# Kernel tuning notes

Hardware: AMD Instinct MI355X
Metric: run time of the kernel (lower is better)

## Reference

```python
import jax, jax.numpy as jnp
import numpy as np

N = 100000


def gcn_conv(x, edge_index, W, b):
    """PyG GCNConv: add self-loops, symmetric normalization, x @ W, aggregate, + bias."""
    n = x.shape[0]
    src = jnp.concatenate([edge_index[0], jnp.arange(n)])
    dst = jnp.concatenate([edge_index[1], jnp.arange(n)])
    deg = jax.ops.segment_sum(jnp.ones_like(dst, dtype=x.dtype), dst, num_segments=n)
    dinv = jnp.where(deg > 0, jax.lax.rsqrt(deg), 0.0)
    norm = dinv[src] * dinv[dst]  # [E+N]
    h = x @ W  # [N, out]
    msg = h[src] * norm[:, None]  # gather + scale
    agg = jax.ops.segment_sum(msg, dst, num_segments=n)
    return agg + b


def setup_inputs() -> dict:
    key = jax.random.key(0)
    ks = jax.random.split(key, 10)
    x = jax.random.normal(ks[0], (N, 256), dtype=jnp.float32)
    edge_index = jax.random.randint(ks[1], (2, 3200000), 0, N, dtype=jnp.int64)
    def glorot(k, fan_in, fan_out):
        s = np.sqrt(6.0 / (fan_in + fan_out)).astype(np.float32)
        return jax.random.uniform(k, (fan_in, fan_out), jnp.float32, -s, s)
    return {
        "x": x,
        "edge_index": edge_index,
        "W1": glorot(ks[2], 256, 128), "b1": jnp.zeros((128,), jnp.float32),
        "W2": glorot(ks[3], 128, 64), "b2": jnp.zeros((64,), jnp.float32),
        "W3": glorot(ks[4], 64, 16), "b3": jnp.zeros((16,), jnp.float32),
        "Wc": glorot(ks[5], 16, 2), "bc": jnp.zeros((2,), jnp.float32),
    }


def reference(x, edge_index, W1, b1, W2, b2, W3, b3, Wc, bc):
    h = jnp.tanh(gcn_conv(x, edge_index, W1, b1))
    h = jnp.tanh(gcn_conv(h, edge_index, W2, b2))
    h = jnp.tanh(gcn_conv(h, edge_index, W3, b3))
    out = h @ Wc + bc
    return (out, h)
```

## Files before the change

### kernel.cpp

```cpp
#include <hip/hip_runtime.h>
#include <hip/hip_fp16.h>
#include <cstdint>
#include <cstddef>


#define EPB 16384
#define BSHIFT 8
#define NBUC_MAX 512
#define BCAP 12800

typedef __attribute__((ext_vector_type(8))) short short8;
typedef __attribute__((ext_vector_type(4))) float f32x4;

__global__ __launch_bounds__(256) void scan_block(const int* __restrict__ src, int n,
                                                  int* __restrict__ incl,
                                                  int* __restrict__ bsum) {
    int tid = threadIdx.x;
    int v = blockIdx.x * 256 + tid;
    int val = (v < n) ? src[v] : 0;
    int lane = tid & 63, w = tid >> 6;
#pragma unroll
    for (int off = 1; off < 64; off <<= 1) {
        int t = __shfl_up(val, off, 64);
        if (lane >= off) val += t;
    }
    __shared__ int wsum[4];
    if (lane == 63) wsum[w] = val;
    __syncthreads();
#pragma unroll
    for (int i = 0; i < 4; ++i)
        if (i < w) val += wsum[i];
    if (v < n) incl[v] = val;
    if (tid == 255) bsum[blockIdx.x] = val;
}

__global__ __launch_bounds__(512) void scan_sums(int* __restrict__ bsum, int nb) {
    int tid = threadIdx.x;
    int val = (tid < nb) ? bsum[tid] : 0;
    int lane = tid & 63, w = tid >> 6;
#pragma unroll
    for (int off = 1; off < 64; off <<= 1) {
        int t = __shfl_up(val, off, 64);
        if (lane >= off) val += t;
    }
    __shared__ int wsum[8];
    if (lane == 63) wsum[w] = val;
    __syncthreads();
#pragma unroll
    for (int i = 0; i < 8; ++i)
        if (i < w) val += wsum[i];
    if (tid < nb) bsum[tid] = val;
}

__global__ __launch_bounds__(256) void finalize_scan(
    const int* __restrict__ incl, const int* __restrict__ bsum,
    const int* __restrict__ src, int n, int* __restrict__ excl) {
    int v = blockIdx.x * 256 + threadIdx.x;
    if (v >= n) return;
    int boff = (blockIdx.x == 0) ? 0 : bsum[blockIdx.x - 1];
    excl[v] = boff + incl[v] - src[v];
}

__global__ __launch_bounds__(256) void hist_bucket(
    const int* __restrict__ ei, int E, int nbuc, int nch,
    int* __restrict__ histG) {
    __shared__ int h[NBUC_MAX];
    const int k = blockIdx.x;
    for (int b = threadIdx.x; b < NBUC_MAX; b += 256) h[b] = 0;
    __syncthreads();
    const int base = k * EPB, end = min(E, base + EPB);
    for (int i = base + threadIdx.x; i < end; i += 256)
        atomicAdd(&h[ei[(size_t)E + i] >> BSHIFT], 1);
    __syncthreads();
    for (int b = threadIdx.x; b < nbuc; b += 256)
        histG[(size_t)b * nch + k] = h[b];
}

__global__ __launch_bounds__(256) void bucket_scatter(
    const int* __restrict__ ei, int E, int nbuc, int nch,
    const int* __restrict__ offs, unsigned int* __restrict__ ebuf) {
    __shared__ int cur[NBUC_MAX];
    const int k = blockIdx.x;
    for (int b = threadIdx.x; b < nbuc; b += 256)
        cur[b] = offs[(size_t)b * nch + k];
    __syncthreads();
    const int base = k * EPB, end = min(E, base + EPB);
    for (int i = base + threadIdx.x; i < end; i += 256) {
        int s = ei[i];
        int d = ei[(size_t)E + i];
        int pos = atomicAdd(&cur[d >> BSHIFT], 1);
        ebuf[pos] = (unsigned)s | ((unsigned)(d & 255) << 24);
    }
}

__global__ __launch_bounds__(256) void bucket_build(
    const unsigned int* __restrict__ ebuf, const int* __restrict__ offs,
    int E, int nbuc, int nch, int n,
    int* __restrict__ col, int* __restrict__ deg,
    int* __restrict__ row_start, float* __restrict__ dinv) {
    const int b = blockIdx.x;
    const int tid = threadIdx.x;
    const int estart = offs[(size_t)b * nch];
    const int eend = (b + 1 < nbuc) ? offs[(size_t)(b + 1) * nch] : E;
    const int cnt = eend - estart;

    __shared__ int degl[256];
    __shared__ int curl[256];
    __shared__ int wsum[4];
    __shared__ int colstage[BCAP];

    degl[tid] = 0;
    __syncthreads();
    for (int i = tid; i < cnt; i += 256)
        atomicAdd(&degl[ebuf[estart + i] >> 24], 1);
    __syncthreads();
    int myDeg = degl[tid];
    int val = myDeg;
    int lane = tid & 63, w = tid >> 6;
#pragma unroll
    for (int off = 1; off < 64; off <<= 1) {
        int t = __shfl_up(val, off, 64);
        if (lane >= off) val += t;
    }
    if (lane == 63) wsum[w] = val;
    __syncthreads();
#pragma unroll
    for (int i = 0; i < 4; ++i)
        if (i < w) val += wsum[i];
    int excl = val - myDeg;
    curl[tid] = excl;
    int v = (b << BSHIFT) + tid;
    if (v < n) {
        deg[v] = myDeg;
        row_start[v] = estart + excl;
        dinv[v] = rsqrtf((float)(myDeg + 1));
    }
    __syncthreads();
    if (cnt <= BCAP) {
        for (int i = tid; i < cnt; i += 256) {
            unsigned int e = ebuf[estart + i];
            int pos = atomicAdd(&curl[e >> 24], 1);
            colstage[pos] = (int)(e & 0xFFFFFFu);
        }
        __syncthreads();
        for (int i = tid; i < cnt; i += 256)
            col[estart + i] = colstage[i];
    } else {
        for (int i = tid; i < cnt; i += 256) {
            unsigned int e = ebuf[estart + i];
            int pos = atomicAdd(&curl[e >> 24], 1);
            col[estart + pos] = (int)(e & 0xFFFFFFu);
        }
    }
}

__device__ inline unsigned short f32_to_bf16_rn(float f) {
    unsigned int u = __float_as_uint(f);
    unsigned int r = (u + 0x7FFFu + ((u >> 16) & 1u)) >> 16;
    return (unsigned short)r;
}
__device__ inline float bf16_to_f32(unsigned short h) {
    return __uint_as_float(((unsigned int)h) << 16);
}

template <int FIN, int FOUT>
__global__ __launch_bounds__(256) void pack_w(const float* __restrict__ W,
                                              unsigned short* __restrict__ Wpk) {
    constexpr int KC = FIN / 32, CF = FOUT / 16;
    constexpr int TOT = KC * CF * 64 * 8;
    int idx = blockIdx.x * 256 + threadIdx.x;
    if (idx >= TOT) return;
    int j = idx & 7;
    int lane = (idx >> 3) & 63;
    int cf = (idx >> 9) % CF;
    int kc = (idx >> 9) / CF;
    int k = kc * 32 + ((lane >> 4) * 8) + j;
    int c = cf * 16 + (lane & 15);
    float w = W[(size_t)k * FOUT + c];
    unsigned short h = f32_to_bf16_rn(w);
    unsigned short l = f32_to_bf16_rn(w - bf16_to_f32(h));
    size_t base = ((size_t)((kc * CF + cf) * 64 + lane)) * 16;
    Wpk[base + j] = h;
    Wpk[base + 8 + j] = l;
}

template <int FIN, int FOUT>
__global__ __launch_bounds__(256) void gemm_mfma(
    const float* __restrict__ X, const unsigned short* __restrict__ Wpk,
    const float* __restrict__ dinv, __half* __restrict__ Hs, int n) {
    constexpr int KC = FIN / 32, CF = FOUT / 16;
    constexpr int BM = 4 * 16;
    const int w = threadIdx.x >> 6, lane = threadIdx.x & 63;
    const int g = lane >> 4, rr = lane & 15;
    const int node0 = blockIdx.x * BM + w * 16;
    const int ko = g * 8;

    f32x4 acc[CF];
#pragma unroll
    for (int cf = 0; cf < CF; ++cf)
        acc[cf] = (f32x4){0.f, 0.f, 0.f, 0.f};

    union U16 { uint4 u; short8 s; };

#pragma unroll 2
    for (int kc = 0; kc < KC; ++kc) {
        short8 ahi, alo;
        {
            int r = node0 + rr;
            float xv[8] = {0.f, 0.f, 0.f, 0.f, 0.f, 0.f, 0.f, 0.f};
            if (r < n) {
                const float* xp = X + (size_t)r * FIN + kc * 32 + ko;
                float4 a0 = *(const float4*)xp;
                float4 a1 = *(const float4*)(xp + 4);
                xv[0] = a0.x; xv[1] = a0.y; xv[2] = a0.z; xv[3] = a0.w;
                xv[4] = a1.x; xv[5] = a1.y; xv[6] = a1.z; xv[7] = a1.w;
            }
#pragma unroll
            for (int j = 0; j < 8; ++j) {
                unsigned int u = __float_as_uint(xv[j]);
                ahi[j] = (short)(unsigned short)(u >> 16);
                float hf = __uint_as_float(u & 0xFFFF0000u);
                alo[j] = (short)f32_to_bf16_rn(xv[j] - hf);
            }
        }
#pragma unroll
        for (int cf = 0; cf < CF; ++cf) {
            const uint4* bp = (const uint4*)(Wpk +
                ((size_t)((kc * CF + cf) * 64 + lane)) * 16);
            U16 bh, bl;
            bh.u = bp[0];
            bl.u = bp[1];
            acc[cf] = __builtin_amdgcn_mfma_f32_16x16x32_bf16(
                ahi, bh.s, acc[cf], 0, 0, 0);
            acc[cf] = __builtin_amdgcn_mfma_f32_16x16x32_bf16(
                alo, bh.s, acc[cf], 0, 0, 0);
            acc[cf] = __builtin_amdgcn_mfma_f32_16x16x32_bf16(
                ahi, bl.s, acc[cf], 0, 0, 0);
        }
    }

#pragma unroll
    for (int i = 0; i < 4; ++i) {
        int r = node0 + g * 4 + i;
        if (r >= n) continue;
        float di = dinv[r];
        __half* hp = Hs + (size_t)r * FOUT + rr;
#pragma unroll
        for (int cf = 0; cf < CF; ++cf)
            hp[cf * 16] = __float2half_rn(acc[cf][i] * di);
    }
}

template <int FIN, int FOUT, int TM>
__global__ __launch_bounds__(256) void gemm_tile_h(
    const float* __restrict__ X, const float* __restrict__ W,
    const float* __restrict__ dinv, __half* __restrict__ Hs, int n) {
    constexpr int CT = FOUT / 4;
    constexpr int RG = 256 / CT;
    static_assert(TM == RG * 4, "tile mismatch");
    constexpr int LROW = FIN + 4;
    __shared__ float xs[TM][LROW];

    const int node0 = blockIdx.x * TM;
    const int tid = threadIdx.x;

    constexpr int C4 = FIN / 4;
    for (int i = tid; i < TM * C4; i += 256) {
        int r = i / C4, c = (i % C4) * 4;
        float4 v = make_float4(0.f, 0.f, 0.f, 0.f);
        if (node0 + r < n) v = *(const float4*)(X + (size_t)(node0 + r) * FIN + c);
        *(float4*)&xs[r][c] = v;
    }
    __syncthreads();

    const int col = (tid % CT) * 4;
    const int r0 = (tid / CT) * 4;

    float acc[4][4];
#pragma unroll
    for (int i = 0; i < 4; ++i)
#pragma unroll
        for (int j = 0; j < 4; ++j) acc[i][j] = 0.f;

#pragma unroll 2
    for (int k = 0; k < FIN; k += 4) {
        float4 w0 = *(const float4*)(W + (size_t)(k + 0) * FOUT + col);
        float4 w1 = *(const float4*)(W + (size_t)(k + 1) * FOUT + col);
        float4 w2 = *(const float4*)(W + (size_t)(k + 2) * FOUT + col);
        float4 w3 = *(const float4*)(W + (size_t)(k + 3) * FOUT + col);
        float4 av[4];
        av[0] = *(const float4*)&xs[r0 + 0][k];
        av[1] = *(const float4*)&xs[r0 + 1][k];
        av[2] = *(const float4*)&xs[r0 + 2][k];
        av[3] = *(const float4*)&xs[r0 + 3][k];
#pragma unroll
        for (int rr = 0; rr < 4; ++rr) {
            acc[rr][0] = fmaf(av[rr].x, w0.x, acc[rr][0]);
            acc[rr][1] = fmaf(av[rr].x, w0.y, acc[rr][1]);
            acc[rr][2] = fmaf(av[rr].x, w0.z, acc[rr][2]);
            acc[rr][3] = fmaf(av[rr].x, w0.w, acc[rr][3]);
            acc[rr][0] = fmaf(av[rr].y, w1.x, acc[rr][0]);
            acc[rr][1] = fmaf(av[rr].y, w1.y, acc[rr][1]);
            acc[rr][2] = fmaf(av[rr].y, w1.z, acc[rr][2]);
            acc[rr][3] = fmaf(av[rr].y, w1.w, acc[rr][3]);
            acc[rr][0] = fmaf(av[rr].z, w2.x, acc[rr][0]);
            acc[rr][1] = fmaf(av[rr].z, w2.y, acc[rr][1]);
            acc[rr][2] = fmaf(av[rr].z, w2.z, acc[rr][2]);
            acc[rr][3] = fmaf(av[rr].z, w2.w, acc[rr][3]);
            acc[rr][0] = fmaf(av[rr].w, w3.x, acc[rr][0]);
            acc[rr][1] = fmaf(av[rr].w, w3.y, acc[rr][1]);
            acc[rr][2] = fmaf(av[rr].w, w3.z, acc[rr][2]);
            acc[rr][3] = fmaf(av[rr].w, w3.w, acc[rr][3]);
        }
    }

#pragma unroll
    for (int rr = 0; rr < 4; ++rr) {
        int node = node0 + r0 + rr;
        if (node < n) {
            float di = dinv[node];
            __half h0 = __float2half_rn(acc[rr][0] * di);
            __half h1 = __float2half_rn(acc[rr][1] * di);
            __half h2 = __float2half_rn(acc[rr][2] * di);
            __half h3 = __float2half_rn(acc[rr][3] * di);
            unsigned short u0 = *(unsigned short*)&h0, u1 = *(unsigned short*)&h1;
            unsigned short u2 = *(unsigned short*)&h2, u3 = *(unsigned short*)&h3;
            uint2 pk;
            pk.x = (unsigned)u0 | ((unsigned)u1 << 16);
            pk.y = (unsigned)u2 | ((unsigned)u3 << 16);
            *(uint2*)(Hs + (size_t)node * FOUT + col) = pk;
        }
    }
}

__device__ inline void add8h(float* acc, uint4 p) {
    unsigned int w[4] = {p.x, p.y, p.z, p.w};
#pragma unroll
    for (int t = 0; t < 4; ++t) {
        __half2 h = *(const __half2*)&w[t];
        float2 f = __half22float2(h);
        acc[2 * t] += f.x;
        acc[2 * t + 1] += f.y;
    }
}

template <int F>
__global__ __launch_bounds__(256) void pull_agg_h(
    const int* __restrict__ row_start, const int* __restrict__ deg,
    const int* __restrict__ col, const __half* __restrict__ Hs,
    const float* __restrict__ dinv, const float* __restrict__ B,
    float* __restrict__ OUT, int n) {
    constexpr int TPE = F / 8;
    long long gid = (long long)blockIdx.x * 256 + threadIdx.x;
    int node = (int)(gid / TPE);
    int lane = (int)(gid % TPE);
    if (node >= n) return;
    const int beg = row_start[node];
    const int cnt = deg[node];
    const size_t lo = (size_t)lane * 8;

    float acc[8] = {0.f, 0.f, 0.f, 0.f, 0.f, 0.f, 0.f, 0.f};
    add8h(acc, *(const uint4*)(Hs + (size_t)node * F + lo));

    int j = 0;
    for (; j + 16 <= cnt; j += 16) {
        int s[16];
#pragma unroll
        for (int t = 0; t < 16; ++t) s[t] = col[beg + j + t];
        uint4 p[16];
#pragma unroll
        for (int t = 0; t < 16; ++t)
            p[t] = *(const uint4*)(Hs + (size_t)s[t] * F + lo);
#pragma unroll
        for (int t = 0; t < 16; ++t) add8h(acc, p[t]);
    }
    for (; j + 8 <= cnt; j += 8) {
        int s[8];
#pragma unroll
        for (int t = 0; t < 8; ++t) s[t] = col[beg + j + t];
        uint4 p[8];
#pragma unroll
        for (int t = 0; t < 8; ++t)
            p[t] = *(const uint4*)(Hs + (size_t)s[t] * F + lo);
#pragma unroll
        for (int t = 0; t < 8; ++t) add8h(acc, p[t]);
    }
    for (; j < cnt; ++j) {
        int s = col[beg + j];
        add8h(acc, *(const uint4*)(Hs + (size_t)s * F + lo));
    }

    float di = dinv[node];
    float4 b0 = *(const float4*)(B + lo);
    float4 b1 = *(const float4*)(B + lo + 4);
    float4 r0, r1;
    r0.x = tanhf(fmaf(acc[0], di, b0.x));
    r0.y = tanhf(fmaf(acc[1], di, b0.y));
    r0.z = tanhf(fmaf(acc[2], di, b0.z));
    r0.w = tanhf(fmaf(acc[3], di, b0.w));
    r1.x = tanhf(fmaf(acc[4], di, b1.x));
    r1.y = tanhf(fmaf(acc[5], di, b1.y));
    r1.z = tanhf(fmaf(acc[6], di, b1.z));
    r1.w = tanhf(fmaf(acc[7], di, b1.w));
    float* op = OUT + (size_t)node * F + lo;
    *(float4*)(op) = r0;
    *(float4*)(op + 4) = r1;
}

__global__ __launch_bounds__(256) void pull_cls(
    const int* __restrict__ row_start, const int* __restrict__ deg,
    const int* __restrict__ col, const __half* __restrict__ Hs,
    const float* __restrict__ dinv, const float* __restrict__ B,
    const float* __restrict__ Wc, const float* __restrict__ bc,
    float* __restrict__ OUTH, float* __restrict__ OUTC, int n) {
    int gid = blockIdx.x * 256 + threadIdx.x;
    int node = gid >> 1;
    if (node >= n) return;
    const int half = gid & 1;
    const size_t lo = (size_t)half * 8;
    const int beg = row_start[node];
    const int cnt = deg[node];

    float acc[8] = {0.f, 0.f, 0.f, 0.f, 0.f, 0.f, 0.f, 0.f};
    add8h(acc, *(const uint4*)(Hs + (size_t)node * 16 + lo));

    int j = 0;
    for (; j + 16 <= cnt; j += 16) {
        int s[16];
#pragma unroll
        for (int t = 0; t < 16; ++t) s[t] = col[beg + j + t];
        uint4 p[16];
#pragma unroll
        for (int t = 0; t < 16; ++t)
            p[t] = *(const uint4*)(Hs + (size_t)s[t] * 16 + lo);
#pragma unroll
        for (int t = 0; t < 16; ++t) add8h(acc, p[t]);
    }
    for (; j + 8 <= cnt; j += 8) {
        int s[8];
#pragma unroll
        for (int t = 0; t < 8; ++t) s[t] = col[beg + j + t];
        uint4 p[8];
#pragma unroll
        for (int t = 0; t < 8; ++t)
            p[t] = *(const uint4*)(Hs + (size_t)s[t] * 16 + lo);
#pragma unroll
        for (int t = 0; t < 8; ++t) add8h(acc, p[t]);
    }
    for (; j < cnt; ++j) {
        int s = col[beg + j];
        add8h(acc, *(const uint4*)(Hs + (size_t)s * 16 + lo));
    }

    float di = dinv[node];
    float r[8];
#pragma unroll
    for (int k = 0; k < 8; ++k)
        r[k] = tanhf(fmaf(acc[k], di, B[lo + k]));

    float* op = OUTH + (size_t)node * 16 + lo;
    *(float4*)(op)     = make_float4(r[0], r[1], r[2], r[3]);
    *(float4*)(op + 4) = make_float4(r[4], r[5], r[6], r[7]);

    float o0 = 0.f, o1 = 0.f;
#pragma unroll
    for (int k = 0; k < 8; ++k) {
        o0 = fmaf(r[k], Wc[(lo + k) * 2 + 0], o0);
        o1 = fmaf(r[k], Wc[(lo + k) * 2 + 1], o1);
    }
    o0 += __shfl_xor(o0, 1);
    o1 += __shfl_xor(o1, 1);
    if (half == 0) {
        OUTC[(size_t)node * 2 + 0] = o0 + bc[0];
        OUTC[(size_t)node * 2 + 1] = o1 + bc[1];
    }
}

extern "C" void kernel_launch(void* const* d_in, const int* in_sizes, int n_in,
                              void* d_out, int out_size, void* d_ws, size_t ws_size,
                              hipStream_t stream) {
    const float* x  = (const float*)d_in[0];
    const int* ei   = (const int*)d_in[1];
    const float* W1 = (const float*)d_in[2];
    const float* b1 = (const float*)d_in[3];
    const float* W2 = (const float*)d_in[4];
    const float* b2 = (const float*)d_in[5];
    const float* W3 = (const float*)d_in[6];
    const float* b3 = (const float*)d_in[7];
    const float* Wc = (const float*)d_in[8];
    const float* bc = (const float*)d_in[9];

    const int n = in_sizes[0] / 256;
    const int E = in_sizes[1] / 2;
    const int nbuc = (n + 255) >> BSHIFT;
    const int nch  = (E + EPB - 1) / EPB;
    const int NH   = nbuc * nch;
    const int nb2  = (NH + 255) / 256;

    float* outp = (float*)d_out;
    float* outh = outp + (size_t)n * 2;

    int*    deg       = (int*)d_ws;
    float*  dinv      = (float*)d_ws + (size_t)n;
    int*    row_start = (int*)d_ws + 2 * (size_t)n;
    int*    histG     = (int*)d_ws + 3 * (size_t)n;
    int*    incl      = histG + NH;
    int*    bsum      = incl + NH;
    int*    offs      = bsum + 512;
    int*    col       = offs + NH;
    __half* HsH       = (__half*)(col + E);
    float*  xbuf      = (float*)(HsH + (size_t)n * 128);
    unsigned int* ebuf = (unsigned int*)xbuf;

    unsigned short* Wpk1 = (unsigned short*)histG;
    unsigned short* Wpk2 = Wpk1 + (size_t)256 * 128 * 2;

    hist_bucket<<<nch, 256, 0, stream>>>(ei, E, nbuc, nch, histG);
    scan_block<<<nb2, 256, 0, stream>>>(histG, NH, incl, bsum);
    scan_sums<<<1, 512, 0, stream>>>(bsum, nb2);
    finalize_scan<<<nb2, 256, 0, stream>>>(incl, bsum, histG, NH, offs);
    bucket_scatter<<<nch, 256, 0, stream>>>(ei, E, nbuc, nch, offs, ebuf);
    bucket_build<<<nbuc, 256, 0, stream>>>(ebuf, offs, E, nbuc, nch, n,
                                           col, deg, row_start, dinv);

    pack_w<256, 128><<<(256 / 32 * 128 / 16 * 512 + 255) / 256, 256, 0, stream>>>(W1, Wpk1);
    pack_w<128, 64><<<(128 / 32 * 64 / 16 * 512 + 255) / 256, 256, 0, stream>>>(W2, Wpk2);

    gemm_mfma<256, 128><<<(n + 63) / 64, 256, 0, stream>>>(x, Wpk1, dinv, HsH, n);
    pull_agg_h<128><<<(int)(((long long)n * 16 + 255) / 256), 256, 0, stream>>>(
        row_start, deg, col, HsH, dinv, b1, xbuf, n);

    gemm_mfma<128, 64><<<(n + 63) / 64, 256, 0, stream>>>(xbuf, Wpk2, dinv, HsH, n);
    pull_agg_h<64><<<(int)(((long long)n * 8 + 255) / 256), 256, 0, stream>>>(
        row_start, deg, col, HsH, dinv, b2, xbuf, n);

    gemm_tile_h<64, 16, 256><<<(n + 255) / 256, 256, 0, stream>>>(xbuf, W3, dinv, HsH, n);
    pull_cls<<<(2 * n + 255) / 256, 256, 0, stream>>>(row_start, deg, col, HsH,
                                                      dinv, b3, Wc, bc, outh, outp, n);
}
```

Before: 634.7 us.

## Sort CSR neighbors and aggregate in source-column chunks for gather locality

Each node's neighbor list is sorted with an in-shared-memory insertion sort in bucket_build, and per-chunk row offsets (chunks of 8192 source nodes) are recorded in a new rsC array. The aggregation kernels are replaced by pull_chunk, where each thread handles several nodes and sweeps all source chunks in the same order. The aim is to keep the working set of gathered feature rows cache-resident across the grid. The cost is a serial per-thread sort in the build kernel, extra offset storage and reads, and lower memory-level parallelism per thread from the smaller unroll. pull_cls also has its unroll trimmed.

```diff
diff --git a/kernel.cpp b/kernel.cpp
--- a/kernel.cpp
+++ b/kernel.cpp
@@ -8,6 +8,7 @@
 #define BSHIFT 8
 #define NBUC_MAX 512
 #define BCAP 12800
+#define CSH 13
 
 typedef __attribute__((ext_vector_type(8))) short short8;
 typedef __attribute__((ext_vector_type(4))) float f32x4;
@@ -95,9 +96,10 @@
 
 __global__ __launch_bounds__(256) void bucket_build(
     const unsigned int* __restrict__ ebuf, const int* __restrict__ offs,
-    int E, int nbuc, int nch, int n,
+    int E, int nbuc, int nch, int n, int NC,
     int* __restrict__ col, int* __restrict__ deg,
-    int* __restrict__ row_start, float* __restrict__ dinv) {
+    int* __restrict__ row_start, float* __restrict__ dinv,
+    int* __restrict__ rsC) {
     const int b = blockIdx.x;
     const int tid = threadIdx.x;
     const int estart = offs[(size_t)b * nch];
@@ -143,6 +145,23 @@
             colstage[pos] = (int)(e & 0xFFFFFFu);
         }
         __syncthreads();
+        for (int a = excl + 1; a < excl + myDeg; ++a) {
+            int key = colstage[a];
+            int p = a - 1;
+            while (p >= excl && colstage[p] > key) {
+                colstage[p + 1] = colstage[p];
+                --p;
+            }
+            colstage[p + 1] = key;
+        }
+        if (v < n) {
+            int idx = 0;
+            for (int c = 0; c < NC; ++c) {
+                rsC[(size_t)c * n + v] = estart + excl + idx;
+                while (idx < myDeg && (colstage[excl + idx] >> CSH) == c) ++idx;
+            }
+        }
+        __syncthreads();
         for (int i = tid; i < cnt; i += 256)
             col[estart + i] = colstage[i];
     } else {
@@ -150,6 +169,11 @@
             unsigned int e = ebuf[estart + i];
             int pos = atomicAdd(&curl[e >> 24], 1);
             col[estart + pos] = (int)(e & 0xFFFFFFu);
+        }
+        if (v < n) {
+            rsC[v] = estart + excl;
+            for (int c = 1; c < NC; ++c)
+                rsC[(size_t)c * n + v] = estart + excl + myDeg;
         }
     }
 }
@@ -344,67 +368,83 @@
     }
 }
 
-template <int F>
-__global__ __launch_bounds__(256) void pull_agg_h(
-    const int* __restrict__ row_start, const int* __restrict__ deg,
-    const int* __restrict__ col, const __half* __restrict__ Hs,
-    const float* __restrict__ dinv, const float* __restrict__ B,
-    float* __restrict__ OUT, int n) {
+template <int F, int NPT>
+__global__ __launch_bounds__(256) void pull_chunk(
+    const int* __restrict__ rsC, const int* __restrict__ row_start,
+    const int* __restrict__ deg, const int* __restrict__ col,
+    const __half* __restrict__ Hs, const float* __restrict__ dinv,
+    const float* __restrict__ B, float* __restrict__ OUT, int n, int NC) {
     constexpr int TPE = F / 8;
-    long long gid = (long long)blockIdx.x * 256 + threadIdx.x;
-    int node = (int)(gid / TPE);
-    int lane = (int)(gid % TPE);
-    if (node >= n) return;
-    const int beg = row_start[node];
-    const int cnt = deg[node];
-    const size_t lo = (size_t)lane * 8;
-
-    float acc[8] = {0.f, 0.f, 0.f, 0.f, 0.f, 0.f, 0.f, 0.f};
-    add8h(acc, *(const uint4*)(Hs + (size_t)node * F + lo));
-
-    int j = 0;
-    for (; j + 16 <= cnt; j += 16) {
-        int s[16];
-#pragma unroll
-        for (int t = 0; t < 16; ++t) s[t] = col[beg + j + t];
-        uint4 p[16];
-#pragma unroll
-        for (int t = 0; t < 16; ++t)
-            p[t] = *(const uint4*)(Hs + (size_t)s[t] * F + lo);
-#pragma unroll
-        for (int t = 0; t < 16; ++t) add8h(acc, p[t]);
-    }
-    for (; j + 8 <= cnt; j += 8) {
-        int s[8];
-#pragma unroll
-        for (int t = 0; t < 8; ++t) s[t] = col[beg + j + t];
-        uint4 p[8];
-#pragma unroll
-        for (int t = 0; t < 8; ++t)
-            p[t] = *(const uint4*)(Hs + (size_t)s[t] * F + lo);
-#pragma unroll
-        for (int t = 0; t < 8; ++t) add8h(acc, p[t]);
-    }
-    for (; j < cnt; ++j) {
-        int s = col[beg + j];
-        add8h(acc, *(const uint4*)(Hs + (size_t)s * F + lo));
-    }
-
-    float di = dinv[node];
-    float4 b0 = *(const float4*)(B + lo);
-    float4 b1 = *(const float4*)(B + lo + 4);
-    float4 r0, r1;
-    r0.x = tanhf(fmaf(acc[0], di, b0.x));
-    r0.y = tanhf(fmaf(acc[1], di, b0.y));
-    r0.z = tanhf(fmaf(acc[2], di, b0.z));
-    r0.w = tanhf(fmaf(acc[3], di, b0.w));
-    r1.x = tanhf(fmaf(acc[4], di, b1.x));
-    r1.y = tanhf(fmaf(acc[5], di, b1.y));
-    r1.z = tanhf(fmaf(acc[6], di, b1.z));
-    r1.w = tanhf(fmaf(acc[7], di, b1.w));
-    float* op = OUT + (size_t)node * F + lo;
-    *(float4*)(op) = r0;
-    *(float4*)(op + 4) = r1;
+    const int T = blockIdx.x * 256 + threadIdx.x;
+    const int STEP = (int)gridDim.x * 256;
+
+    float acc[NPT][8];
+#pragma unroll
+    for (int i = 0; i < NPT; ++i)
+#pragma unroll
+        for (int k = 0; k < 8; ++k) acc[i][k] = 0.f;
+
+#pragma unroll
+    for (int i = 0; i < NPT; ++i) {
+        int gid = T + i * STEP;
+        int node = gid / TPE;
+        if (node < n) {
+            int lane = gid & (TPE - 1);
+            add8h(acc[i], *(const uint4*)(Hs + (size_t)node * F + lane * 8));
+        }
+    }
+
+    for (int c = 0; c < NC; ++c) {
+#pragma unroll
+        for (int i = 0; i < NPT; ++i) {
+            int gid = T + i * STEP;
+            int node = gid / TPE;
+            if (node >= n) continue;
+            int lane = gid & (TPE - 1);
+            const size_t lo = (size_t)lane * 8;
+            int j = rsC[(size_t)c * n + node];
+            int end = (c + 1 < NC) ? rsC[(size_t)(c + 1) * n + node]
+                                   : row_start[node] + deg[node];
+            for (; j + 4 <= end; j += 4) {
+                int s0 = col[j + 0], s1 = col[j + 1];
+                int s2 = col[j + 2], s3 = col[j + 3];
+                uint4 p0 = *(const uint4*)(Hs + (size_t)s0 * F + lo);
+                uint4 p1 = *(const uint4*)(Hs + (size_t)s1 * F + lo);
+                uint4 p2 = *(const uint4*)(Hs + (size_t)s2 * F + lo);
+                uint4 p3 = *(const uint4*)(Hs + (size_t)s3 * F + lo);
+                add8h(acc[i], p0); add8h(acc[i], p1);
+                add8h(acc[i], p2); add8h(acc[i], p3);
+            }
+            for (; j < end; ++j) {
+                int s = col[j];
+                add8h(acc[i], *(const uint4*)(Hs + (size_t)s * F + lo));
+            }
+        }
+    }
+
+#pragma unroll
+    for (int i = 0; i < NPT; ++i) {
+        int gid = T + i * STEP;
+        int node = gid / TPE;
+        if (node >= n) continue;
+        int lane = gid & (TPE - 1);
+        const size_t lo = (size_t)lane * 8;
+        float di = dinv[node];
+        float4 b0 = *(const float4*)(B + lo);
+        float4 b1 = *(const float4*)(B + lo + 4);
+        float4 r0, r1;
+        r0.x = tanhf(fmaf(acc[i][0], di, b0.x));
+        r0.y = tanhf(fmaf(acc[i][1], di, b0.y));
+        r0.z = tanhf(fmaf(acc[i][2], di, b0.z));
+        r0.w = tanhf(fmaf(acc[i][3], di, b0.w));
+        r1.x = tanhf(fmaf(acc[i][4], di, b1.x));
+        r1.y = tanhf(fmaf(acc[i][5], di, b1.y));
+        r1.z = tanhf(fmaf(acc[i][6], di, b1.z));
+        r1.w = tanhf(fmaf(acc[i][7], di, b1.w));
+        float* op = OUT + (size_t)node * F + lo;
+        *(float4*)(op) = r0;
+        *(float4*)(op + 4) = r1;
+    }
 }
 
 __global__ __launch_bounds__(256) void pull_cls(
@@ -425,27 +465,21 @@
     add8h(acc, *(const uint4*)(Hs + (size_t)node * 16 + lo));
 
     int j = 0;
-    for (; j + 16 <= cnt; j += 16) {
-        int s[16];
-#pragma unroll
-        for (int t = 0; t < 16; ++t) s[t] = col[beg + j + t];
-        uint4 p[16];
-#pragma unroll
-        for (int t = 0; t < 16; ++t)
-            p[t] = *(const uint4*)(Hs + (size_t)s[t] * 16 + lo);
-#pragma unroll
-        for (int t = 0; t < 16; ++t) add8h(acc, p[t]);
-    }
     for (; j + 8 <= cnt; j += 8) {
-        int s[8];
-#pragma unroll
-        for (int t = 0; t < 8; ++t) s[t] = col[beg + j + t];
-        uint4 p[8];
-#pragma unroll
-        for (int t = 0; t < 8; ++t)
-            p[t] = *(const uint4*)(Hs + (size_t)s[t] * 16 + lo);
-#pragma unroll
-        for (int t = 0; t < 8; ++t) add8h(acc, p[t]);
+        int s0 = col[beg + j + 0], s1 = col[beg + j + 1];
+        int s2 = col[beg + j + 2], s3 = col[beg + j + 3];
+        int s4 = col[beg + j + 4], s5 = col[beg + j + 5];
+        int s6 = col[beg + j + 6], s7 = col[beg + j + 7];
+        uint4 p0 = *(const uint4*)(Hs + (size_t)s0 * 16 + lo);
+        uint4 p1 = *(const uint4*)(Hs + (size_t)s1 * 16 + lo);
+        uint4 p2 = *(const uint4*)(Hs + (size_t)s2 * 16 + lo);
+        uint4 p3 = *(const uint4*)(Hs + (size_t)s3 * 16 + lo);
+        uint4 p4 = *(const uint4*)(Hs + (size_t)s4 * 16 + lo);
+        uint4 p5 = *(const uint4*)(Hs + (size_t)s5 * 16 + lo);
+        uint4 p6 = *(const uint4*)(Hs + (size_t)s6 * 16 + lo);
+        uint4 p7 = *(const uint4*)(Hs + (size_t)s7 * 16 + lo);
+        add8h(acc, p0); add8h(acc, p1); add8h(acc, p2); add8h(acc, p3);
+        add8h(acc, p4); add8h(acc, p5); add8h(acc, p6); add8h(acc, p7);
     }
     for (; j < cnt; ++j) {
         int s = col[beg + j];
@@ -496,6 +530,7 @@
     const int nch  = (E + EPB - 1) / EPB;
     const int NH   = nbuc * nch;
     const int nb2  = (NH + 255) / 256;
+    const int NC   = (n + (1 << CSH) - 1) >> CSH;
 
     float* outp = (float*)d_out;
     float* outh = outp + (size_t)n * 2;
@@ -510,6 +545,7 @@
     int*    col       = offs + NH;
     __half* HsH       = (__half*)(col + E);
     float*  xbuf      = (float*)(HsH + (size_t)n * 128);
+    int*    rsC       = (int*)(xbuf + (size_t)n * 128);
     unsigned int* ebuf = (unsigned int*)xbuf;
 
     unsigned short* Wpk1 = (unsigned short*)histG;
@@ -520,19 +556,22 @@
     scan_sums<<<1, 512, 0, stream>>>(bsum, nb2);
     finalize_scan<<<nb2, 256, 0, stream>>>(incl, bsum, histG, NH, offs);
     bucket_scatter<<<nch, 256, 0, stream>>>(ei, E, nbuc, nch, offs, ebuf);
-    bucket_build<<<nbuc, 256, 0, stream>>>(ebuf, offs, E, nbuc, nch, n,
-                                           col, deg, row_start, dinv);
+    bucket_build<<<nbuc, 256, 0, stream>>>(ebuf, offs, E, nbuc, nch, n, NC,
+                                           col, deg, row_start, dinv, rsC);
 
     pack_w<256, 128><<<(256 / 32 * 128 / 16 * 512 + 255) / 256, 256, 0, stream>>>(W1, Wpk1);
     pack_w<128, 64><<<(128 / 32 * 64 / 16 * 512 + 255) / 256, 256, 0, stream>>>(W2, Wpk2);
 
+    const int G1 = (n + 127) / 128;
+    const int G2 = (n + 127) / 128;
+
     gemm_mfma<256, 128><<<(n + 63) / 64, 256, 0, stream>>>(x, Wpk1, dinv, HsH, n);
-    pull_agg_h<128><<<(int)(((long long)n * 16 + 255) / 256), 256, 0, stream>>>(
-        row_start, deg, col, HsH, dinv, b1, xbuf, n);
+    pull_chunk<128, 8><<<G1, 256, 0, stream>>>(rsC, row_start, deg, col, HsH,
+                                               dinv, b1, xbuf, n, NC);
 
     gemm_mfma<128, 64><<<(n + 63) / 64, 256, 0, stream>>>(xbuf, Wpk2, dinv, HsH, n);
-    pull_agg_h<64><<<(int)(((long long)n * 8 + 255) / 256), 256, 0, stream>>>(
-        row_start, deg, col, HsH, dinv, b2, xbuf, n);
+    pull_chunk<64, 4><<<G2, 256, 0, stream>>>(rsC, row_start, deg, col, HsH,
+                                              dinv, b2, xbuf, n, NC);
 
     gemm_tile_h<64, 16, 256><<<(n + 255) / 256, 256, 0, stream>>>(xbuf, W3, dinv, HsH, n);
     pull_cls<<<(2 * n + 255) / 256, 256, 0, stream>>>(row_start, deg, col, HsH,
```

Result: slower. 1.112 ms (+75.2%).

## Stage packed weights in double-buffered swizzled LDS and compute two row tiles per wave

Applied to the files above, without the earlier changes.

The MFMA GEMM kernel now copies each K-slice of the packed hi/lo bf16 weights into a double-buffered shared-memory buffer. The slices are written in an XOR-swizzled layout, and pack_w is changed to produce that layout. Each wave processes two 16-row tiles and reuses each weight fragment across both, so blocks cover 128 rows and the grid is halved. This is meant to cut repeated global/L2 weight loads per MFMA. In exchange it adds LDS use, a barrier per K-step, and more accumulator registers, which may lower occupancy.

```diff
diff --git a/kernel.cpp b/kernel.cpp
--- a/kernel.cpp
+++ b/kernel.cpp
@@ -163,10 +163,15 @@
     return __uint_as_float(((unsigned int)h) << 16);
 }
 
+__device__ __host__ inline int swz(int a) {
+    return a ^ (((a >> 7) & 3) << 4);
+}
+
 template <int FIN, int FOUT>
 __global__ __launch_bounds__(256) void pack_w(const float* __restrict__ W,
                                               unsigned short* __restrict__ Wpk) {
     constexpr int KC = FIN / 32, CF = FOUT / 16;
+    constexpr int SLICE = CF * 64 * 16;
     constexpr int TOT = KC * CF * 64 * 8;
     int idx = blockIdx.x * 256 + threadIdx.x;
     if (idx >= TOT) return;
@@ -179,34 +184,58 @@
     float w = W[(size_t)k * FOUT + c];
     unsigned short h = f32_to_bf16_rn(w);
     unsigned short l = f32_to_bf16_rn(w - bf16_to_f32(h));
-    size_t base = ((size_t)((kc * CF + cf) * 64 + lane)) * 16;
-    Wpk[base + j] = h;
-    Wpk[base + 8 + j] = l;
+    int ah = (cf * 64 + lane) * 32 + j * 2;
+    int al = ah + 16;
+    Wpk[(size_t)kc * SLICE + (swz(ah) >> 1)] = h;
+    Wpk[(size_t)kc * SLICE + (swz(al) >> 1)] = l;
 }
 
 template <int FIN, int FOUT>
 __global__ __launch_bounds__(256) void gemm_mfma(
     const float* __restrict__ X, const unsigned short* __restrict__ Wpk,
     const float* __restrict__ dinv, __half* __restrict__ Hs, int n) {
-    constexpr int KC = FIN / 32, CF = FOUT / 16;
-    constexpr int BM = 4 * 16;
-    const int w = threadIdx.x >> 6, lane = threadIdx.x & 63;
+    constexpr int KC = FIN / 32, CF = FOUT / 16, RF = 2;
+    constexpr int BM = 4 * RF * 16;
+    constexpr int SLICE = CF * 64 * 16;
+    constexpr int NV = SLICE / 8;
+    __shared__ __align__(16) unsigned short bsh[2 * SLICE];
+
+    const int tid = threadIdx.x;
+    const int w = tid >> 6, lane = tid & 63;
     const int g = lane >> 4, rr = lane & 15;
-    const int node0 = blockIdx.x * BM + w * 16;
+    const int node0 = blockIdx.x * BM + w * (RF * 16);
     const int ko = g * 8;
 
-    f32x4 acc[CF];
-#pragma unroll
-    for (int cf = 0; cf < CF; ++cf)
-        acc[cf] = (f32x4){0.f, 0.f, 0.f, 0.f};
+    f32x4 acc[RF][CF];
+#pragma unroll
+    for (int rf = 0; rf < RF; ++rf)
+#pragma unroll
+        for (int cf = 0; cf < CF; ++cf)
+            acc[rf][cf] = (f32x4){0.f, 0.f, 0.f, 0.f};
 
     union U16 { uint4 u; short8 s; };
 
-#pragma unroll 2
+    {
+        const uint4* src = (const uint4*)Wpk;
+        uint4* dst = (uint4*)bsh;
+#pragma unroll
+        for (int i = 0; i < NV / 256; ++i) dst[i * 256 + tid] = src[i * 256 + tid];
+    }
+    __syncthreads();
+
+#pragma unroll
     for (int kc = 0; kc < KC; ++kc) {
-        short8 ahi, alo;
-        {
-            int r = node0 + rr;
+        if (kc + 1 < KC) {
+            const uint4* src = (const uint4*)(Wpk + (size_t)(kc + 1) * SLICE);
+            uint4* dst = (uint4*)(bsh + ((kc + 1) & 1) * SLICE);
+#pragma unroll
+            for (int i = 0; i < NV / 256; ++i) dst[i * 256 + tid] = src[i * 256 + tid];
+        }
+
+        short8 ahi[RF], alo[RF];
+#pragma unroll
+        for (int rf = 0; rf < RF; ++rf) {
+            int r = node0 + rf * 16 + rr;
             float xv[8] = {0.f, 0.f, 0.f, 0.f, 0.f, 0.f, 0.f, 0.f};
             if (r < n) {
                 const float* xp = X + (size_t)r * FIN + kc * 32 + ko;
@@ -218,36 +247,46 @@
 #pragma unroll
             for (int j = 0; j < 8; ++j) {
                 unsigned int u = __float_as_uint(xv[j]);
-                ahi[j] = (short)(unsigned short)(u >> 16);
+                ahi[rf][j] = (short)(unsigned short)(u >> 16);
                 float hf = __uint_as_float(u & 0xFFFF0000u);
-                alo[j] = (short)f32_to_bf16_rn(xv[j] - hf);
+                alo[rf][j] = (short)f32_to_bf16_rn(xv[j] - hf);
             }
         }
+
+        const char* bufp = (const char*)(bsh + (kc & 1) * SLICE);
 #pragma unroll
         for (int cf = 0; cf < CF; ++cf) {
-            const uint4* bp = (const uint4*)(Wpk +
-                ((size_t)((kc * CF + cf) * 64 + lane)) * 16);
+            int a0 = (cf * 64 + lane) * 32;
+            int ash = swz(a0);
+            int asl = swz(a0 + 16);
             U16 bh, bl;
-            bh.u = bp[0];
-            bl.u = bp[1];
-            acc[cf] = __builtin_amdgcn_mfma_f32_16x16x32_bf16(
-                ahi, bh.s, acc[cf], 0, 0, 0);
-            acc[cf] = __builtin_amdgcn_mfma_f32_16x16x32_bf16(
-                alo, bh.s, acc[cf], 0, 0, 0);
-            acc[cf] = __builtin_amdgcn_mfma_f32_16x16x32_bf16(
-                ahi, bl.s, acc[cf], 0, 0, 0);
-        }
-    }
-
-#pragma unroll
-    for (int i = 0; i < 4; ++i) {
-        int r = node0 + g * 4 + i;
-        if (r >= n) continue;
-        float di = dinv[r];
-        __half* hp = Hs + (size_t)r * FOUT + rr;
-#pragma unroll
-        for (int cf = 0; cf < CF; ++cf)
-            hp[cf * 16] = __float2half_rn(acc[cf][i] * di);
+            bh.u = *(const uint4*)(bufp + ash);
+            bl.u = *(const uint4*)(bufp + asl);
+#pragma unroll
+            for (int rf = 0; rf < RF; ++rf) {
+                acc[rf][cf] = __builtin_amdgcn_mfma_f32_16x16x32_bf16(
+                    ahi[rf], bh.s, acc[rf][cf], 0, 0, 0);
+                acc[rf][cf] = __builtin_amdgcn_mfma_f32_16x16x32_bf16(
+                    alo[rf], bh.s, acc[rf][cf], 0, 0, 0);
+                acc[rf][cf] = __builtin_amdgcn_mfma_f32_16x16x32_bf16(
+                    ahi[rf], bl.s, acc[rf][cf], 0, 0, 0);
+            }
+        }
+        __syncthreads();
+    }
+
+#pragma unroll
+    for (int rf = 0; rf < RF; ++rf) {
+#pragma unroll
+        for (int i = 0; i < 4; ++i) {
+            int r = node0 + rf * 16 + g * 4 + i;
+            if (r >= n) continue;
+            float di = dinv[r];
+            __half* hp = Hs + (size_t)r * FOUT + rr;
+#pragma unroll
+            for (int cf = 0; cf < CF; ++cf)
+                hp[cf * 16] = __float2half_rn(acc[rf][cf][i] * di);
+        }
     }
 }
 
@@ -526,11 +565,11 @@
     pack_w<256, 128><<<(256 / 32 * 128 / 16 * 512 + 255) / 256, 256, 0, stream>>>(W1, Wpk1);
     pack_w<128, 64><<<(128 / 32 * 64 / 16 * 512 + 255) / 256, 256, 0, stream>>>(W2, Wpk2);
 
-    gemm_mfma<256, 128><<<(n + 63) / 64, 256, 0, stream>>>(x, Wpk1, dinv, HsH, n);
+    gemm_mfma<256, 128><<<(n + 127) / 128, 256, 0, stream>>>(x, Wpk1, dinv, HsH, n);
     pull_agg_h<128><<<(int)(((long long)n * 16 + 255) / 256), 256, 0, stream>>>(
         row_start, deg, col, HsH, dinv, b1, xbuf, n);
 
-    gemm_mfma<128, 64><<<(n + 63) / 64, 256, 0, stream>>>(xbuf, Wpk2, dinv, HsH, n);
+    gemm_mfma<128, 64><<<(n + 127) / 128, 256, 0, stream>>>(xbuf, Wpk2, dinv, HsH, n);
     pull_agg_h<64><<<(int)(((long long)n * 8 + 255) / 256), 256, 0, stream>>>(
         row_start, deg, col, HsH, dinv, b2, xbuf, n);
 
```

Measured after the change: 611.5 us. -3.7%, faster.
